# Optimization experiments

Hardware: AMD Instinct MI355X
Metric: run time of the kernel (lower is better)

The kernel has to match this reference:

```python
import jax, jax.numpy as jnp
import numpy as np

FIELD = 32
DIM = 64
LAYER_SIZE = (128, 128)


def setup_inputs() -> dict:
    key = jax.random.key(0)
    ks = jax.random.split(key, 5)
    B = 4096
    x = jax.random.normal(ks[0], (B, FIELD, DIM), dtype=jnp.float32)
    # conv1d kernel-size-1 weights, stored as [out_channels, in_channels]
    field_nums = [FIELD]
    params = {}
    for i, size in enumerate(LAYER_SIZE):
        in_ch = field_nums[-1] * field_nums[0]
        fan = 1.0 / np.sqrt(in_ch)
        params[f"w{i}"] = jax.random.uniform(ks[1 + 2 * i % 4], (size, in_ch), minval=-fan, maxval=fan, dtype=jnp.float32)
        params[f"b{i}"] = jax.random.uniform(ks[2 + 2 * i % 4], (size,), minval=-fan, maxval=fan, dtype=jnp.float32)
        field_nums.append(size // 2)
    return {"cin_inputs": x, "w0": params["w0"], "b0": params["b0"], "w1": params["w1"], "b1": params["b1"]}


def _cin(x, weights, biases):
    # x: [B, F, D]
    B, F, D = x.shape
    hidden = x
    finals = []
    n_layers = len(weights)
    for i, (w, b) in enumerate(zip(weights, biases)):
        size = w.shape[0]
        # outer product over field dims: [B, H, F, D] -> reshape to [B, H*F, D]
        z = jnp.einsum('bhd,bfd->bhfd', hidden, x).reshape(B, hidden.shape[1] * F, D)
        # 1x1 conv over channel dim == per-position matmul
        y = jnp.einsum('bcd,oc->bod', z, w) + b[None, :, None]
        y = jax.nn.relu(y)
        if i != n_layers - 1:
            hidden, direct = y[:, : size // 2, :], y[:, size // 2 :, :]
        else:
            direct = y
        finals.append(direct)
    return jnp.concatenate(finals, axis=1).sum(-1)  # [B, out_dim]


def reference(cin_inputs, w0, b0, w1, b1):
    return _cin(cin_inputs, [w0, w1], [b0, b1])
```

## Files before the change

kernel.cpp:

```cpp
#include <hip/hip_runtime.h>
#include <hip/hip_fp16.h>


typedef __attribute__((ext_vector_type(8))) _Float16 f16x8;
typedef __attribute__((ext_vector_type(4))) float f32x4;
typedef __attribute__((ext_vector_type(4))) unsigned short us4;
typedef unsigned short ushortT;

__global__ void cin_pack_w(const float* __restrict__ w0,
                           const float* __restrict__ w1,
                           ushortT* __restrict__ wp) {
    int gidx = blockIdx.x * 256 + threadIdx.x;
    if (gidx >= 49152) return;
    const float* src;
    ushortT* dst;
    if (gidx < 16384) {
        int kk = gidx >> 9, rem = gidx & 511;
        int n = rem >> 6, lp = rem & 63;
        int o = n * 16 + (lp & 15);
        int c = kk * 32 + ((lp >> 4) << 3);
        src = w0 + o * 1024 + c;
        dst = wp + gidx * 8;
    } else {
        int g1 = gidx - 16384;
        int kk = g1 >> 9, rem = g1 & 511;
        int n = rem >> 6, lp = rem & 63;
        int o = n * 16 + (lp & 15);
        int c = kk * 32 + ((lp >> 4) << 3);
        src = w1 + o * 2048 + c;
        dst = wp + 131072 + g1 * 8;
    }
    ushortT tmp[8];
#pragma unroll
    for (int j = 0; j < 8; ++j) {
        __half h = __float2half(src[j]);
        tmp[j] = __builtin_bit_cast(ushortT, h);
    }
    *reinterpret_cast<f16x8*>(dst) = *reinterpret_cast<const f16x8*>(tmp);
}

__global__ __launch_bounds__(256, 2) void cin_mfma_kernel(
    const float* __restrict__ x,
    const float* __restrict__ b0,
    const float* __restrict__ b1,
    const ushortT* __restrict__ wp,
    float* __restrict__ out)
{
    const int tid = threadIdx.x;
    const int l   = tid & 63;
    const int w   = tid >> 6;
    const int b   = blockIdx.x * 4 + w;
    const int r16 = l & 15;
    const int g   = l >> 4;

    __shared__ ushortT U[4][4096];
    __shared__ __align__(16) ushortT Wb[2][8192];

    ushortT* Xw = U[w];

    const float* xb = x + (size_t)b * 2048;
#pragma unroll
    for (int i = 0; i < 8; ++i) {
        float4 v = reinterpret_cast<const float4*>(xb)[i * 64 + l];
        int flat = (i * 64 + l) * 4;
        us4 h;
        h[0] = __builtin_bit_cast(ushortT, __float2half(v.x));
        h[1] = __builtin_bit_cast(ushortT, __float2half(v.y));
        h[2] = __builtin_bit_cast(ushortT, __float2half(v.z));
        h[3] = __builtin_bit_cast(ushortT, __float2half(v.w));
        *reinterpret_cast<us4*>(&Xw[flat]) = h;
    }

#pragma unroll
    for (int j = 0; j < 4; ++j) {
        const int seg = w * 4 + j;
        const char* src = (const char*)wp + (size_t)seg * 1024 + (size_t)l * 16;
        __builtin_amdgcn_global_load_lds((const unsigned int*)src,
                                         (unsigned int*)&Wb[0][seg * 512], 16, 0, 0);
    }
    __syncthreads();

    __half2 tf16[4][4];
#pragma unroll
    for (int mt = 0; mt < 4; ++mt)
#pragma unroll
        for (int p = 0; p < 4; ++p) {
            unsigned lo = Xw[(g * 8 + 2 * p) * 64 + mt * 16 + r16];
            unsigned hi = Xw[(g * 8 + 2 * p + 1) * 64 + mt * 16 + r16];
            tf16[mt][p] = __builtin_bit_cast(__half2, lo | (hi << 16));
        }

    f32x4 acc[4][8];
#pragma unroll
    for (int mt = 0; mt < 4; ++mt)
#pragma unroll
        for (int n = 0; n < 8; ++n) acc[mt][n] = (f32x4){0.f, 0.f, 0.f, 0.f};

    union AfU { __half2 h2[4]; f16x8 v; };

#pragma unroll 1
    for (int p = 0; p < 48; ++p) {
        const int ps = p & 1;
        const int k0 = 2 * p;

        if (p + 1 < 48) {
#pragma unroll
            for (int j = 0; j < 4; ++j) {
                const int seg = w * 4 + j;
                const char* src = (const char*)wp + (size_t)(p + 1) * 16384 +
                                  (size_t)seg * 1024 + (size_t)l * 16;
                __builtin_amdgcn_global_load_lds((const unsigned int*)src,
                    (unsigned int*)&Wb[ps ^ 1][seg * 512], 16, 0, 0);
            }
        }

        const ushortT* th0p = Xw + (size_t)((k0 < 32) ? k0 : (k0 - 32)) * 64;
        __half2 th[4];
#pragma unroll
        for (int mt = 0; mt < 4; ++mt) {
            unsigned u = th0p[mt * 16 + r16];
            th[mt] = __builtin_bit_cast(__half2, (u << 16) | u);
        }

        f16x8 Bf[8];
#pragma unroll
        for (int n = 0; n < 8; ++n)
            Bf[n] = *reinterpret_cast<const f16x8*>(&Wb[ps][n * 512 + l * 8]);

        AfU Af[4];
#pragma unroll
        for (int mt = 0; mt < 4; ++mt)
#pragma unroll
            for (int q = 0; q < 4; ++q)
                Af[mt].h2[q] = __hmul2(tf16[mt][q], th[mt]);

        const int k1 = k0 + 1;
        const ushortT* th1p = Xw + (size_t)((k1 < 32) ? k1 : (k1 - 32)) * 64;
#pragma unroll
        for (int mt = 0; mt < 4; ++mt) {
            unsigned u = th1p[mt * 16 + r16];
            th[mt] = __builtin_bit_cast(__half2, (u << 16) | u);
        }

        __builtin_amdgcn_s_setprio(1);
#pragma unroll
        for (int n = 0; n < 8; ++n) {
#pragma unroll
            for (int mt = 0; mt < 4; ++mt)
                acc[mt][n] = __builtin_amdgcn_mfma_f32_16x16x32_f16(
                    Af[mt].v, Bf[n], acc[mt][n], 0, 0, 0);
            Bf[n] = *reinterpret_cast<const f16x8*>(&Wb[ps][4096 + n * 512 + l * 8]);
        }
        __builtin_amdgcn_s_setprio(0);

#pragma unroll
        for (int mt = 0; mt < 4; ++mt)
#pragma unroll
            for (int q = 0; q < 4; ++q)
                Af[mt].h2[q] = __hmul2(tf16[mt][q], th[mt]);

        __builtin_amdgcn_s_setprio(1);
#pragma unroll
        for (int n = 0; n < 8; ++n)
#pragma unroll
            for (int mt = 0; mt < 4; ++mt)
                acc[mt][n] = __builtin_amdgcn_mfma_f32_16x16x32_f16(
                    Af[mt].v, Bf[n], acc[mt][n], 0, 0, 0);
        __builtin_amdgcn_s_setprio(0);

        __syncthreads();

        if (p == 15) {
            ushortT* Hw = Xw;
#pragma unroll
            for (int n = 0; n < 4; ++n) {
                float bn = b0[n * 16 + r16];
#pragma unroll
                for (int mt = 0; mt < 4; ++mt) {
                    us4 hv;
#pragma unroll
                    for (int r = 0; r < 4; ++r) {
                        float y = fmaxf(acc[mt][n][r] + bn, 0.f);
                        hv[r] = __builtin_bit_cast(ushortT, __float2half(y));
                    }
                    const int o = n * 16 + r16;
                    *reinterpret_cast<us4*>(&Hw[o * 64 + mt * 16 + g * 4]) = hv;
                }
            }
#pragma unroll
            for (int n = 4; n < 8; ++n) {
                float bn = b0[n * 16 + r16];
                float s = 0.f;
#pragma unroll
                for (int mt = 0; mt < 4; ++mt)
#pragma unroll
                    for (int r = 0; r < 4; ++r)
                        s += fmaxf(acc[mt][n][r] + bn, 0.f);
                s += __shfl_xor(s, 16);
                s += __shfl_xor(s, 32);
                if (l < 16) out[(size_t)b * 192 + (n - 4) * 16 + l] = s;
            }
#pragma unroll
            for (int mt = 0; mt < 4; ++mt)
#pragma unroll
                for (int n = 0; n < 8; ++n) acc[mt][n] = (f32x4){0.f, 0.f, 0.f, 0.f};
        }
    }

#pragma unroll
    for (int n = 0; n < 8; ++n) {
        float bn = b1[n * 16 + r16];
        float s = 0.f;
#pragma unroll
        for (int mt = 0; mt < 4; ++mt)
#pragma unroll
            for (int r = 0; r < 4; ++r)
                s += fmaxf(acc[mt][n][r] + bn, 0.f);
        s += __shfl_xor(s, 16);
        s += __shfl_xor(s, 32);
        if (l < 16) out[(size_t)b * 192 + 64 + n * 16 + l] = s;
    }
}

__global__ __launch_bounds__(256, 4) void cin_fp32_kernel(
    const float* __restrict__ x, const float* __restrict__ w0,
    const float* __restrict__ b0, const float* __restrict__ w1,
    const float* __restrict__ b1, float* __restrict__ out)
{
    const int b = blockIdx.x;
    const int tid = threadIdx.x;
    const int d = tid & 63;
    const int wave = tid >> 6;

    __shared__ float Xs[32][64];
    __shared__ float Hsf[64][64];

    const float* xb = x + (size_t)b * 2048;
    float treg[32];
#pragma unroll
    for (int f = 0; f < 32; ++f) treg[f] = xb[f * 64 + d];
    if (wave == 0) {
#pragma unroll
        for (int f = 0; f < 32; ++f) Xs[f][d] = treg[f];
    }
    __syncthreads();
    const int o_base = __builtin_amdgcn_readfirstlane(wave * 32);

    for (int oi = 0; oi < 32; ++oi) {
        const int o = o_base + oi;
        const float* wrow = w0 + (size_t)o * 1024;
        float acc = b0[o];
        for (int h = 0; h < 32; ++h) {
            const float* wv = wrow + h * 32;
            const float th = Xs[h][d];
            float s0 = 0.f, s1 = 0.f, s2 = 0.f, s3 = 0.f;
#pragma unroll
            for (int f = 0; f < 32; f += 4) {
                s0 = fmaf(wv[f + 0], treg[f + 0], s0);
                s1 = fmaf(wv[f + 1], treg[f + 1], s1);
                s2 = fmaf(wv[f + 2], treg[f + 2], s2);
                s3 = fmaf(wv[f + 3], treg[f + 3], s3);
            }
            acc = fmaf((s0 + s1) + (s2 + s3), th, acc);
        }
        float y = fmaxf(acc, 0.f);
        if (o < 64) {
            Hsf[o][d] = y;
        } else {
#pragma unroll
            for (int off = 32; off > 0; off >>= 1) y += __shfl_xor(y, off, 64);
            if (d == 0) out[(size_t)b * 192 + (o - 64)] = y;
        }
    }
    __syncthreads();

    for (int oi = 0; oi < 32; ++oi) {
        const int o = o_base + oi;
        const float* wrow = w1 + (size_t)o * 2048;
        float acc = b1[o];
        for (int h = 0; h < 64; ++h) {
            const float* wv = wrow + h * 32;
            const float th = Hsf[h][d];
            float s0 = 0.f, s1 = 0.f, s2 = 0.f, s3 = 0.f;
#pragma unroll
            for (int f = 0; f < 32; f += 4) {
                s0 = fmaf(wv[f + 0], treg[f + 0], s0);
                s1 = fmaf(wv[f + 1], treg[f + 1], s1);
                s2 = fmaf(wv[f + 2], treg[f + 2], s2);
                s3 = fmaf(wv[f + 3], treg[f + 3], s3);
            }
            acc = fmaf((s0 + s1) + (s2 + s3), th, acc);
        }
        float y = fmaxf(acc, 0.f);
#pragma unroll
        for (int off = 32; off > 0; off >>= 1) y += __shfl_xor(y, off, 64);
        if (d == 0) out[(size_t)b * 192 + 64 + o] = y;
    }
}

extern "C" void kernel_launch(void* const* d_in, const int* in_sizes, int n_in,
                              void* d_out, int out_size, void* d_ws, size_t ws_size,
                              hipStream_t stream) {
    const float* x  = (const float*)d_in[0];
    const float* w0 = (const float*)d_in[1];
    const float* b0 = (const float*)d_in[2];
    const float* w1 = (const float*)d_in[3];
    const float* b1 = (const float*)d_in[4];
    float* out = (float*)d_out;

    if (ws_size >= 786432) {
        ushortT* wp = (ushortT*)d_ws;
        cin_pack_w<<<192, 256, 0, stream>>>(w0, w1, wp);
        cin_mfma_kernel<<<1024, 256, 0, stream>>>(x, b0, b1, wp, out);
    } else {
        cin_fp32_kernel<<<4096, 256, 0, stream>>>(x, w0, b0, w1, b1, out);
    }
}
```

Baseline: 162.5 us.

## Switch CIN matmul to 32x32x16 MFMA tiles with padded hidden layout

Replaces the 16x16x32 f16 MFMA tiling with 32x32x16 MFMA instructions, repacking the weight layout and restructuring the A-fragment build and accumulators to match. The hidden-state buffer written after layer 0 uses a padded row stride of 68 to reduce LDS bank conflicts on the scattered stores. The aim is fewer MFMA issues and fewer LDS operand loads per FLOP, in exchange for a larger per-wave LDS footprint and a different register layout for the accumulators.

```diff
diff --git a/kernel.cpp b/kernel.cpp
--- a/kernel.cpp
+++ b/kernel.cpp
@@ -3,7 +3,7 @@
 
 
 typedef __attribute__((ext_vector_type(8))) _Float16 f16x8;
-typedef __attribute__((ext_vector_type(4))) float f32x4;
+typedef __attribute__((ext_vector_type(16))) float f32x16;
 typedef __attribute__((ext_vector_type(4))) unsigned short us4;
 typedef unsigned short ushortT;
 
@@ -12,24 +12,17 @@
                            ushortT* __restrict__ wp) {
     int gidx = blockIdx.x * 256 + threadIdx.x;
     if (gidx >= 49152) return;
+    int ktg = gidx >> 9;
+    int rem = gidx & 511;
+    int nt  = rem >> 7;
+    int s   = (rem >> 6) & 1;
+    int l   = rem & 63;
+    int o   = nt * 32 + (l & 31);
+    int cb  = s * 16 + ((l >> 5) << 3);
     const float* src;
-    ushortT* dst;
-    if (gidx < 16384) {
-        int kk = gidx >> 9, rem = gidx & 511;
-        int n = rem >> 6, lp = rem & 63;
-        int o = n * 16 + (lp & 15);
-        int c = kk * 32 + ((lp >> 4) << 3);
-        src = w0 + o * 1024 + c;
-        dst = wp + gidx * 8;
-    } else {
-        int g1 = gidx - 16384;
-        int kk = g1 >> 9, rem = g1 & 511;
-        int n = rem >> 6, lp = rem & 63;
-        int o = n * 16 + (lp & 15);
-        int c = kk * 32 + ((lp >> 4) << 3);
-        src = w1 + o * 2048 + c;
-        dst = wp + 131072 + g1 * 8;
-    }
+    if (ktg < 32) src = w0 + (size_t)o * 1024 + ktg * 32 + cb;
+    else          src = w1 + (size_t)o * 2048 + (ktg - 32) * 32 + cb;
+    ushortT* dst = wp + (size_t)gidx * 8;
     ushortT tmp[8];
 #pragma unroll
     for (int j = 0; j < 8; ++j) {
@@ -50,10 +43,10 @@
     const int l   = tid & 63;
     const int w   = tid >> 6;
     const int b   = blockIdx.x * 4 + w;
-    const int r16 = l & 15;
-    const int g   = l >> 4;
-
-    __shared__ ushortT U[4][4096];
+    const int l31 = l & 31;
+    const int g5  = l >> 5;
+
+    __shared__ ushortT U[4][4352];
     __shared__ __align__(16) ushortT Wb[2][8192];
 
     ushortT* Xw = U[w];
@@ -80,21 +73,26 @@
     }
     __syncthreads();
 
-    __half2 tf16[4][4];
-#pragma unroll
-    for (int mt = 0; mt < 4; ++mt)
-#pragma unroll
-        for (int p = 0; p < 4; ++p) {
-            unsigned lo = Xw[(g * 8 + 2 * p) * 64 + mt * 16 + r16];
-            unsigned hi = Xw[(g * 8 + 2 * p + 1) * 64 + mt * 16 + r16];
-            tf16[mt][p] = __builtin_bit_cast(__half2, lo | (hi << 16));
-        }
-
-    f32x4 acc[4][8];
-#pragma unroll
-    for (int mt = 0; mt < 4; ++mt)
-#pragma unroll
-        for (int n = 0; n < 8; ++n) acc[mt][n] = (f32x4){0.f, 0.f, 0.f, 0.f};
+    __half2 tf[2][2][4];
+#pragma unroll
+    for (int mt = 0; mt < 2; ++mt)
+#pragma unroll
+        for (int s = 0; s < 2; ++s)
+#pragma unroll
+            for (int q = 0; q < 4; ++q) {
+                int f0 = s * 16 + g5 * 8 + 2 * q;
+                unsigned lo = Xw[f0 * 64 + mt * 32 + l31];
+                unsigned hi = Xw[(f0 + 1) * 64 + mt * 32 + l31];
+                tf[mt][s][q] = __builtin_bit_cast(__half2, lo | (hi << 16));
+            }
+
+    f32x16 acc[2][4];
+#pragma unroll
+    for (int mt = 0; mt < 2; ++mt)
+#pragma unroll
+        for (int nt = 0; nt < 4; ++nt)
+#pragma unroll
+            for (int r = 0; r < 16; ++r) acc[mt][nt][r] = 0.f;
 
     union AfU { __half2 h2[4]; f16x8 v; };
 
@@ -102,6 +100,7 @@
     for (int p = 0; p < 48; ++p) {
         const int ps = p & 1;
         const int k0 = 2 * p;
+        const int k1 = k0 + 1;
 
         if (p + 1 < 48) {
 #pragma unroll
@@ -114,58 +113,71 @@
             }
         }
 
-        const ushortT* th0p = Xw + (size_t)((k0 < 32) ? k0 : (k0 - 32)) * 64;
-        __half2 th[4];
-#pragma unroll
-        for (int mt = 0; mt < 4; ++mt) {
-            unsigned u = th0p[mt * 16 + r16];
+        const ushortT* th0p = (k0 < 32) ? (Xw + (size_t)k0 * 64)
+                                        : (Xw + (size_t)(k0 - 32) * 68);
+        __half2 th[2];
+#pragma unroll
+        for (int mt = 0; mt < 2; ++mt) {
+            unsigned u = th0p[mt * 32 + l31];
             th[mt] = __builtin_bit_cast(__half2, (u << 16) | u);
         }
 
         f16x8 Bf[8];
 #pragma unroll
-        for (int n = 0; n < 8; ++n)
-            Bf[n] = *reinterpret_cast<const f16x8*>(&Wb[ps][n * 512 + l * 8]);
-
-        AfU Af[4];
-#pragma unroll
-        for (int mt = 0; mt < 4; ++mt)
-#pragma unroll
-            for (int q = 0; q < 4; ++q)
-                Af[mt].h2[q] = __hmul2(tf16[mt][q], th[mt]);
-
-        const int k1 = k0 + 1;
-        const ushortT* th1p = Xw + (size_t)((k1 < 32) ? k1 : (k1 - 32)) * 64;
-#pragma unroll
-        for (int mt = 0; mt < 4; ++mt) {
-            unsigned u = th1p[mt * 16 + r16];
+        for (int nt = 0; nt < 4; ++nt)
+#pragma unroll
+            for (int s = 0; s < 2; ++s)
+                Bf[nt * 2 + s] = *reinterpret_cast<const f16x8*>(
+                    &Wb[ps][nt * 1024 + s * 512 + l * 8]);
+
+        AfU Af[2][2];
+#pragma unroll
+        for (int mt = 0; mt < 2; ++mt)
+#pragma unroll
+            for (int s = 0; s < 2; ++s)
+#pragma unroll
+                for (int q = 0; q < 4; ++q)
+                    Af[mt][s].h2[q] = __hmul2(tf[mt][s][q], th[mt]);
+
+        const ushortT* th1p = (k1 < 32) ? (Xw + (size_t)k1 * 64)
+                                        : (Xw + (size_t)(k1 - 32) * 68);
+#pragma unroll
+        for (int mt = 0; mt < 2; ++mt) {
+            unsigned u = th1p[mt * 32 + l31];
             th[mt] = __builtin_bit_cast(__half2, (u << 16) | u);
         }
 
         __builtin_amdgcn_s_setprio(1);
 #pragma unroll
-        for (int n = 0; n < 8; ++n) {
-#pragma unroll
-            for (int mt = 0; mt < 4; ++mt)
-                acc[mt][n] = __builtin_amdgcn_mfma_f32_16x16x32_f16(
-                    Af[mt].v, Bf[n], acc[mt][n], 0, 0, 0);
-            Bf[n] = *reinterpret_cast<const f16x8*>(&Wb[ps][4096 + n * 512 + l * 8]);
-        }
+        for (int nt = 0; nt < 4; ++nt)
+#pragma unroll
+            for (int s = 0; s < 2; ++s) {
+#pragma unroll
+                for (int mt = 0; mt < 2; ++mt)
+                    acc[mt][nt] = __builtin_amdgcn_mfma_f32_32x32x16_f16(
+                        Af[mt][s].v, Bf[nt * 2 + s], acc[mt][nt], 0, 0, 0);
+                Bf[nt * 2 + s] = *reinterpret_cast<const f16x8*>(
+                    &Wb[ps][4096 + nt * 1024 + s * 512 + l * 8]);
+            }
         __builtin_amdgcn_s_setprio(0);
 
 #pragma unroll
-        for (int mt = 0; mt < 4; ++mt)
-#pragma unroll
-            for (int q = 0; q < 4; ++q)
-                Af[mt].h2[q] = __hmul2(tf16[mt][q], th[mt]);
+        for (int mt = 0; mt < 2; ++mt)
+#pragma unroll
+            for (int s = 0; s < 2; ++s)
+#pragma unroll
+                for (int q = 0; q < 4; ++q)
+                    Af[mt][s].h2[q] = __hmul2(tf[mt][s][q], th[mt]);
 
         __builtin_amdgcn_s_setprio(1);
 #pragma unroll
-        for (int n = 0; n < 8; ++n)
-#pragma unroll
-            for (int mt = 0; mt < 4; ++mt)
-                acc[mt][n] = __builtin_amdgcn_mfma_f32_16x16x32_f16(
-                    Af[mt].v, Bf[n], acc[mt][n], 0, 0, 0);
+        for (int nt = 0; nt < 4; ++nt)
+#pragma unroll
+            for (int s = 0; s < 2; ++s)
+#pragma unroll
+                for (int mt = 0; mt < 2; ++mt)
+                    acc[mt][nt] = __builtin_amdgcn_mfma_f32_32x32x16_f16(
+                        Af[mt][s].v, Bf[nt * 2 + s], acc[mt][nt], 0, 0, 0);
         __builtin_amdgcn_s_setprio(0);
 
         __syncthreads();
@@ -173,52 +185,55 @@
         if (p == 15) {
             ushortT* Hw = Xw;
 #pragma unroll
-            for (int n = 0; n < 4; ++n) {
-                float bn = b0[n * 16 + r16];
-#pragma unroll
-                for (int mt = 0; mt < 4; ++mt) {
-                    us4 hv;
-#pragma unroll
-                    for (int r = 0; r < 4; ++r) {
-                        float y = fmaxf(acc[mt][n][r] + bn, 0.f);
-                        hv[r] = __builtin_bit_cast(ushortT, __float2half(y));
+            for (int nt = 0; nt < 2; ++nt) {
+                float bn = b0[nt * 32 + l31];
+                const int o = nt * 32 + l31;
+#pragma unroll
+                for (int mt = 0; mt < 2; ++mt)
+#pragma unroll
+                    for (int q = 0; q < 4; ++q) {
+                        us4 hv;
+#pragma unroll
+                        for (int r = 0; r < 4; ++r) {
+                            float y = fmaxf(acc[mt][nt][q * 4 + r] + bn, 0.f);
+                            hv[r] = __builtin_bit_cast(ushortT, __float2half(y));
+                        }
+                        const int d = mt * 32 + q * 8 + g5 * 4;
+                        *reinterpret_cast<us4*>(&Hw[o * 68 + d]) = hv;
                     }
-                    const int o = n * 16 + r16;
-                    *reinterpret_cast<us4*>(&Hw[o * 64 + mt * 16 + g * 4]) = hv;
-                }
-            }
-#pragma unroll
-            for (int n = 4; n < 8; ++n) {
-                float bn = b0[n * 16 + r16];
+            }
+#pragma unroll
+            for (int nt = 2; nt < 4; ++nt) {
+                float bn = b0[nt * 32 + l31];
                 float s = 0.f;
 #pragma unroll
-                for (int mt = 0; mt < 4; ++mt)
-#pragma unroll
-                    for (int r = 0; r < 4; ++r)
-                        s += fmaxf(acc[mt][n][r] + bn, 0.f);
-                s += __shfl_xor(s, 16);
+                for (int mt = 0; mt < 2; ++mt)
+#pragma unroll
+                    for (int r = 0; r < 16; ++r)
+                        s += fmaxf(acc[mt][nt][r] + bn, 0.f);
                 s += __shfl_xor(s, 32);
-                if (l < 16) out[(size_t)b * 192 + (n - 4) * 16 + l] = s;
-            }
-#pragma unroll
-            for (int mt = 0; mt < 4; ++mt)
-#pragma unroll
-                for (int n = 0; n < 8; ++n) acc[mt][n] = (f32x4){0.f, 0.f, 0.f, 0.f};
-        }
-    }
-
-#pragma unroll
-    for (int n = 0; n < 8; ++n) {
-        float bn = b1[n * 16 + r16];
+                if (l < 32) out[(size_t)b * 192 + (nt - 2) * 32 + l] = s;
+            }
+#pragma unroll
+            for (int mt = 0; mt < 2; ++mt)
+#pragma unroll
+                for (int nt = 0; nt < 4; ++nt)
+#pragma unroll
+                    for (int r = 0; r < 16; ++r) acc[mt][nt][r] = 0.f;
+        }
+    }
+
+#pragma unroll
+    for (int nt = 0; nt < 4; ++nt) {
+        float bn = b1[nt * 32 + l31];
         float s = 0.f;
 #pragma unroll
-        for (int mt = 0; mt < 4; ++mt)
-#pragma unroll
-            for (int r = 0; r < 4; ++r)
-                s += fmaxf(acc[mt][n][r] + bn, 0.f);
-        s += __shfl_xor(s, 16);
+        for (int mt = 0; mt < 2; ++mt)
+#pragma unroll
+            for (int r = 0; r < 16; ++r)
+                s += fmaxf(acc[mt][nt][r] + bn, 0.f);
         s += __shfl_xor(s, 32);
-        if (l < 16) out[(size_t)b * 192 + 64 + n * 16 + l] = s;
+        if (l < 32) out[(size_t)b * 192 + 64 + nt * 32 + l] = s;
     }
 }
 
```

After: 181.9 us. 11.9% more time.
